# Kernel tuning notes

Measured on AMD Instinct MI355X. Metric: run time of the kernel, lower is better.

The kernel has to match this reference:

```python
import jax, jax.numpy as jnp
import numpy as np

L, D, H, F, V, B, S = 6, 1024, 16, 4096, 32000, 2, 1024
DK = D // H
EPS = 1e-6

def _make_pe(seq, d):
    pos = np.arange(seq)[:, None].astype(np.float32)
    div = np.exp(np.arange(0, d, 2).astype(np.float32) * (-np.log(10000.0) / d))
    pe = np.zeros((seq, d), np.float32)
    pe[:, 0::2] = np.sin(pos * div)
    pe[:, 1::2] = np.cos(pos * div)
    return jnp.asarray(pe)

def setup_inputs() -> dict:
    key = jax.random.key(0)
    ks = jax.random.split(key, 8)
    def xav(k, shape, fi, fo):
        lim = np.sqrt(6.0 / (fi + fo)).astype(np.float32)
        return jax.random.uniform(k, shape, jnp.float32, -lim, lim)
    return {
        "input_ids": jax.random.randint(ks[0], (B, S), 0, V),
        "attention_mask": jnp.ones((B, S), jnp.float32),
        "emb": jax.random.normal(ks[1], (V, D), jnp.float32) * 0.02,
        "pe": _make_pe(S, D),
        "w_q": xav(ks[2], (L, D, D), D, D),
        "w_k": xav(ks[3], (L, D, D), D, D),
        "w_v": xav(ks[4], (L, D, D), D, D),
        "w_o": xav(ks[5], (L, D, D), D, D),
        "b_o": jnp.zeros((L, D), jnp.float32),
        "w1": xav(ks[6], (L, D, F), D, F),
        "b1": jnp.zeros((L, F), jnp.float32),
        "w2": xav(ks[7], (L, F, D), F, D),
        "b2": jnp.zeros((L, D), jnp.float32),
        "ln1_s": jnp.ones((L, D), jnp.float32),
        "ln1_b": jnp.zeros((L, D), jnp.float32),
        "ln2_s": jnp.ones((L, D), jnp.float32),
        "ln2_b": jnp.zeros((L, D), jnp.float32),
        "lnf_s": jnp.ones((D,), jnp.float32),
        "lnf_b": jnp.zeros((D,), jnp.float32),
    }

def _ln(x, s, b):
    m = x.mean(-1, keepdims=True)
    v = jnp.mean((x - m) ** 2, axis=-1, keepdims=True)  # biased var, like torch LayerNorm
    return (x - m) / jnp.sqrt(v + EPS) * s + b

def reference(input_ids, attention_mask, emb, pe, w_q, w_k, w_v, w_o, b_o,
              w1, b1, w2, b2, ln1_s, ln1_b, ln2_s, ln2_b, lnf_s, lnf_b):
    mask = attention_mask[:, None, None, :]          # [B,1,1,S], broadcasts over heads & queries
    x = emb[input_ids] * jnp.sqrt(jnp.float32(D)) + pe[None, :S]   # [B,S,D]

    def heads(h, w):                                 # [B,S,D] -> [B,H,S,DK]
        return (h @ w).reshape(B, S, H, DK).transpose(0, 2, 1, 3)

    def step(x, p):
        wq, wk, wv, wo, bo, W1, B1, W2, B2, s1, c1, s2, c2 = p
        h = _ln(x, s1, c1)                           # pre-norm
        q, k, v = heads(h, wq), heads(h, wk), heads(h, wv)
        scores = jnp.einsum('bhqd,bhkd->bhqk', q, k) / np.sqrt(DK).astype(np.float32)
        scores = jnp.where(mask == 0, -1e9, scores)
        attn = jax.nn.softmax(scores, axis=-1)       # dropout is identity in eval
        out = jnp.einsum('bhqk,bhkd->bhqd', attn, v)
        out = out.transpose(0, 2, 1, 3).reshape(B, S, D) @ wo + bo
        x = x + out
        h2 = _ln(x, s2, c2)
        ff = jax.nn.relu(h2 @ W1 + B1) @ W2 + B2
        return x + ff, None

    x, _ = jax.lax.scan(step, x, (w_q, w_k, w_v, w_o, b_o, w1, b1, w2, b2,
                                  ln1_s, ln1_b, ln2_s, ln2_b))
    return _ln(x, lnf_s, lnf_b)                      # last_hidden_state [B,S,D]
```

## Files before the change

### kernel.cpp

```cpp
#include <hip/hip_runtime.h>
#include <hip/hip_bf16.h>

#define DL 6
#define DD 1024
#define DH 16
#define DF 4096
#define DB 2
#define DS 1024
#define DDK 64

typedef __hip_bfloat16 bf16;
typedef short mfma_t;
typedef mfma_t mfma8 __attribute__((ext_vector_type(8)));
typedef float floatx4 __attribute__((ext_vector_type(4)));

__device__ __forceinline__ float b2f(bf16 v) { return __bfloat162float(v); }
__device__ __forceinline__ bf16 f2b(float v) { return __float2bfloat16(v); }
__device__ __forceinline__ float rd(const void* p, size_t i, int dt) {
  return dt ? b2f(((const bf16*)p)[i]) : ((const float*)p)[i];
}

__device__ __forceinline__ void gld_lds16(const bf16* g, bf16* l) {
  __builtin_amdgcn_global_load_lds(
      (const __attribute__((address_space(1))) unsigned int*)g,
      (__attribute__((address_space(3))) unsigned int*)l, 16, 0, 0);
}

__global__ void detect_dtype(const unsigned* __restrict__ msk, int* __restrict__ flag) {
  if (threadIdx.x == 0) flag[0] = (msk[0] == 0x3F800000u) ? 0 : 1;
}

template <int OP>
__device__ __forceinline__ float block_reduce(float v, float* sm) {
#pragma unroll
  for (int off = 32; off > 0; off >>= 1) {
    float o = __shfl_down(v, off, 64);
    v = OP ? fmaxf(v, o) : v + o;
  }
  if ((threadIdx.x & 63) == 0) sm[threadIdx.x >> 6] = v;
  __syncthreads();
  float r = OP ? fmaxf(fmaxf(sm[0], sm[1]), fmaxf(sm[2], sm[3]))
               : (sm[0] + sm[1]) + (sm[2] + sm[3]);
  __syncthreads();
  return r;
}

__global__ __launch_bounds__(256) void embed_kernel(const int* __restrict__ ids,
                                                    const void* __restrict__ emb,
                                                    const void* __restrict__ pe,
                                                    const int* __restrict__ dflag,
                                                    float* __restrict__ x) {
  const int dt = dflag[0];
  int t = blockIdx.x;
  int id = ids[t];
  int s = t & (DS - 1);
  int c = threadIdx.x * 4;
  float* xo = x + (size_t)t * DD + c;
#pragma unroll
  for (int i = 0; i < 4; ++i)
    xo[i] = rd(emb, (size_t)id * DD + c + i, dt) * 32.0f + rd(pe, (size_t)s * DD + c + i, dt);
}

__global__ __launch_bounds__(256) void ln_kernel(const float* __restrict__ x,
                                                 const void* __restrict__ s,
                                                 const void* __restrict__ b,
                                                 long long poff,
                                                 const int* __restrict__ dflag,
                                                 void* __restrict__ out, int is_final) {
  __shared__ float sm[4];
  const int dt = dflag[0];
  int row = blockIdx.x;
  const float4* xr = (const float4*)(x + (size_t)row * DD);
  float4 v = xr[threadIdx.x];
  float sum = block_reduce<0>(v.x + v.y + v.z + v.w, sm);
  float mean = sum * (1.0f / DD);
  float dx = v.x - mean, dy = v.y - mean, dz = v.z - mean, dw = v.w - mean;
  float ss = block_reduce<0>(dx * dx + dy * dy + dz * dz + dw * dw, sm);
  float rstd = rsqrtf(ss * (1.0f / DD) + 1e-6f);
  int c = threadIdx.x * 4;
  size_t p = (size_t)poff + c;
  float o0 = dx * rstd * rd(s, p + 0, dt) + rd(b, p + 0, dt);
  float o1 = dy * rstd * rd(s, p + 1, dt) + rd(b, p + 1, dt);
  float o2 = dz * rstd * rd(s, p + 2, dt) + rd(b, p + 2, dt);
  float o3 = dw * rstd * rd(s, p + 3, dt) + rd(b, p + 3, dt);
  if (is_final && dt == 0) {
    float* o = (float*)out + (size_t)row * DD + c;
    o[0] = o0; o[1] = o1; o[2] = o2; o[3] = o3;
  } else {
    bf16* o = (bf16*)out + (size_t)row * DD + c;
    o[0] = f2b(o0); o[1] = f2b(o1); o[2] = f2b(o2); o[3] = f2b(o3);
  }
}

__global__ __launch_bounds__(256) void transpose_any(const void* __restrict__ in,
                                                     long long row_off,
                                                     bf16* __restrict__ out,
                                                     int rows, int cols,
                                                     const int* __restrict__ dflag) {
  __shared__ bf16 t[32][33];
  const int dt = dflag[0];
  int c0 = blockIdx.x * 32, r0 = blockIdx.y * 32;
  int tx = threadIdx.x & 31, ty = threadIdx.x >> 5;
#pragma unroll
  for (int i = 0; i < 4; ++i) {
    int r = ty + i * 8;
    size_t idx = (size_t)(row_off + r0 + r) * cols + c0 + tx;
    t[r][tx] = dt ? ((const bf16*)in)[idx] : f2b(((const float*)in)[idx]);
  }
  __syncthreads();
#pragma unroll
  for (int i = 0; i < 4; ++i) {
    int r = ty + i * 8;
    out[(size_t)(c0 + r) * rows + r0 + tx] = t[tx][r];
  }
}

__global__ __launch_bounds__(256) void vtrans_kernel(const bf16* __restrict__ qkv,
                                                     bf16* __restrict__ vt) {
  __shared__ bf16 t[32][33];
  int bh = blockIdx.z;
  const bf16* src = qkv + (size_t)(bh >> 4) * DS * 3072 + 2048 + (bh & 15) * DDK;
  bf16* dst = vt + (size_t)bh * DDK * DS;
  int s0 = blockIdx.x * 32, d0 = blockIdx.y * 32;
  int tx = threadIdx.x & 31, ty = threadIdx.x >> 5;
#pragma unroll
  for (int i = 0; i < 4; ++i) {
    int r = ty + i * 8;
    t[r][tx] = src[(size_t)(s0 + r) * 3072 + d0 + tx];
  }
  __syncthreads();
#pragma unroll
  for (int i = 0; i < 4; ++i) {
    int r = ty + i * 8;
    dst[(size_t)(d0 + r) * DS + s0 + tx] = t[tx][r];
  }
}

#define KVBLK 128
__global__ __launch_bounds__(256) void flash_attn(const bf16* __restrict__ qkv,
                                                  const bf16* __restrict__ vt,
                                                  const void* __restrict__ msk,
                                                  const int* __restrict__ dflag,
                                                  bf16* __restrict__ ao) {
  __shared__ __align__(16) bf16 Qs[64 * 64];
  __shared__ __align__(16) bf16 Ks[KVBLK * 64];
  __shared__ __align__(16) bf16 Vs[64 * KVBLK];
  __shared__ __align__(16) bf16 Ps[4 * 16 * KVBLK];
  __shared__ float Ms[KVBLK];
  __shared__ float Sx[4][16];

  const int tid = threadIdx.x;
  const int lane = tid & 63, wave = tid >> 6;
  const int lane16 = lane & 15, laneq = lane >> 4;
  const int dt = dflag[0];
  const int qt = blockIdx.x, bh = blockIdx.y;
  const int b = bh >> 4, h = bh & 15;
  const int q0 = qt * 64;

  const bf16* Qg = qkv + (size_t)b * DS * 3072 + (size_t)q0 * 3072 + h * 64;
  const bf16* Kg = qkv + (size_t)b * DS * 3072 + 1024 + h * 64;
  const bf16* Vg = vt + (size_t)bh * DDK * DS;

#pragma unroll
  for (int i = 0; i < 2; ++i) {
    int c = tid + i * 256;
    int row = c >> 3, sl = c & 7;
    gld_lds16(Qg + (size_t)row * 3072 + ((sl ^ (row & 7)) << 3), &Qs[c * 8]);
  }
  auto stage = [&](int kv0) {
#pragma unroll
    for (int i = 0; i < 4; ++i) {
      int c = tid + i * 256;
      int row = c >> 3, sl = c & 7;
      gld_lds16(Kg + (size_t)(kv0 + row) * 3072 + ((sl ^ (row & 7)) << 3), &Ks[c * 8]);
    }
#pragma unroll
    for (int i = 0; i < 4; ++i) {
      int c = tid + i * 256;
      int row = c >> 4, sl = c & 15;
      gld_lds16(Vg + (size_t)row * DS + kv0 + ((sl ^ (row & 7)) << 3), &Vs[c * 8]);
    }
    if (tid < KVBLK) Ms[tid] = rd(msk, (size_t)b * DS + kv0 + tid, dt);
  };

  stage(0);
  __syncthreads();

  mfma8 bq[2];
  {
    int qrow = wave * 16 + lane16;
#pragma unroll
    for (int ks = 0; ks < 2; ++ks)
      bq[ks] = *(const mfma8*)(&Qs[qrow * 64 + (((laneq + ks * 4) ^ (qrow & 7)) << 3)]);
  }

  floatx4 acc_o[4];
#pragma unroll
  for (int d = 0; d < 4; ++d) { floatx4 z = {0.f, 0.f, 0.f, 0.f}; acc_o[d] = z; }
  float m_run = -1e30f, l_run = 0.f;

  for (int kv = 0; kv < DS / KVBLK; ++kv) {
    floatx4 s[8];
#pragma unroll
    for (int t = 0; t < 8; ++t) { floatx4 z = {0.f, 0.f, 0.f, 0.f}; s[t] = z; }
#pragma unroll
    for (int ks = 0; ks < 2; ++ks)
#pragma unroll
      for (int t = 0; t < 8; ++t) {
        int krow = t * 16 + lane16;
        mfma8 a = *(const mfma8*)(&Ks[krow * 64 + (((laneq + ks * 4) ^ (krow & 7)) << 3)]);
        s[t] = __builtin_amdgcn_mfma_f32_16x16x32_bf16(a, bq[ks], s[t], 0, 0, 0);
      }
    float pmax = -1e30f;
#pragma unroll
    for (int t = 0; t < 8; ++t) {
      float4 mk = *(const float4*)(&Ms[t * 16 + laneq * 4]);
#pragma unroll
      for (int r = 0; r < 4; ++r) {
        float sv = ((&mk.x)[r] == 0.f) ? -1e9f : s[t][r] * 0.125f;
        s[t][r] = sv;
        pmax = fmaxf(pmax, sv);
      }
    }
    pmax = fmaxf(pmax, __shfl_xor(pmax, 16, 64));
    pmax = fmaxf(pmax, __shfl_xor(pmax, 32, 64));
    float m_new = fmaxf(m_run, pmax);
    float scal = __expf(m_run - m_new);
    float lsum = 0.f;
#pragma unroll
    for (int t = 0; t < 8; ++t)
#pragma unroll
      for (int r = 0; r < 4; ++r) {
        float p = __expf(s[t][r] - m_new);
        s[t][r] = p;
        lsum += p;
      }
    lsum += __shfl_xor(lsum, 16, 64);
    lsum += __shfl_xor(lsum, 32, 64);
    l_run = l_run * scal + lsum;
    m_run = m_new;
    if (laneq == 0) Sx[wave][lane16] = scal;
    {
      int rowb = (wave * 16 + lane16) * 2 * KVBLK;
#pragma unroll
      for (int t = 0; t < 8; ++t) {
        int off = (t * 32 + laneq * 8) ^ ((lane16 & 7) << 4);
        union { bf16 v[4]; uint2 u; } pk;
        pk.v[0] = f2b(s[t][0]); pk.v[1] = f2b(s[t][1]);
        pk.v[2] = f2b(s[t][2]); pk.v[3] = f2b(s[t][3]);
        *(uint2*)((char*)&Ps[0] + rowb + off) = pk.u;
      }
    }
    float4 sc4 = *(const float4*)(&Sx[wave][laneq * 4]);
#pragma unroll
    for (int d = 0; d < 4; ++d)
#pragma unroll
      for (int r = 0; r < 4; ++r) acc_o[d][r] *= (&sc4.x)[r];
#pragma unroll
    for (int ks = 0; ks < 4; ++ks) {
      mfma8 pa = *(const mfma8*)((char*)&Ps[0] + (wave * 16 + lane16) * 2 * KVBLK +
                                 ((ks * 64 + laneq * 16) ^ ((lane16 & 7) << 4)));
#pragma unroll
      for (int d = 0; d < 4; ++d) {
        int drow = d * 16 + lane16;
        mfma8 vb = *(const mfma8*)((char*)&Vs[0] + drow * 2 * KVBLK +
                                   ((ks * 64 + laneq * 16) ^ ((drow & 7) << 4)));
        acc_o[d] = __builtin_amdgcn_mfma_f32_16x16x32_bf16(pa, vb, acc_o[d], 0, 0, 0);
      }
    }
    __syncthreads();
    if (kv + 1 < DS / KVBLK) {
      stage((kv + 1) * KVBLK);
      __syncthreads();
    }
  }

  if (laneq == 0) Sx[wave][lane16] = l_run;
  float4 l4 = *(const float4*)(&Sx[wave][laneq * 4]);
#pragma unroll
  for (int r = 0; r < 4; ++r) {
    float inv = 1.f / (&l4.x)[r];
    int q = q0 + wave * 16 + laneq * 4 + r;
    size_t base = ((size_t)b * DS + q) * DD + h * 64;
#pragma unroll
    for (int d = 0; d < 4; ++d) ao[base + d * 16 + lane16] = f2b(acc_o[d][r] * inv);
  }
}

enum { EPI_BF16 = 0, EPI_BIAS_RELU = 1, EPI_ACC_ATOMIC = 2, EPI_SCORES = 3 };

template <int NT, int WM_, int WN_, int TM, int TN, int EPI>
__global__ __launch_bounds__(256) void gemm_bt(
    const bf16* __restrict__ A, int lda, long long zsa,
    const bf16* __restrict__ Bt, int ldb, long long zsb,
    void* __restrict__ C, int ldc, long long zsc,
    int K, const void* __restrict__ aux, long long aoff, float scale,
    const int* __restrict__ dflag) {
  constexpr int MT = 128, BK = 32;
  constexpr int SM = MT / WM_, SN = NT / WN_;
  constexpr int nsA = (MT * BK / 8) / 256;
  constexpr int nsB = (NT * BK / 8) / 256;
  __shared__ __align__(16) bf16 As[2][MT * BK];
  __shared__ __align__(16) bf16 Bs[2][NT * BK];
  const int tid = threadIdx.x;
  const int lane = tid & 63, wave = tid >> 6;
  const int lane16 = lane & 15, laneq = lane >> 4;
  const int wm = wave / WN_, wn = wave % WN_;
  const int dt = dflag[0];
  const long long z = blockIdx.z;
  A += z * zsa;
  Bt += z * zsb;
  const int m0 = blockIdx.x * MT, n0 = blockIdx.y * NT;

  floatx4 acc[TM][TN];
#pragma unroll
  for (int i = 0; i < TM; ++i)
#pragma unroll
    for (int j = 0; j < TN; ++j) {
      floatx4 zz = {0.f, 0.f, 0.f, 0.f};
      acc[i][j] = zz;
    }

  auto stage = [&](int buf, int k0) {
#pragma unroll
    for (int i = 0; i < nsA; ++i) {
      int c = tid + i * 256;
      int row = c >> 2, kk = (c & 3) << 3;
      gld_lds16(A + (size_t)(m0 + row) * lda + k0 + kk,
                &As[buf][(size_t)(wave * 64 + i * 256) * 8]);
    }
#pragma unroll
    for (int i = 0; i < nsB; ++i) {
      int c = tid + i * 256;
      int row = c >> 2, kk = (c & 3) << 3;
      gld_lds16(Bt + (size_t)(n0 + row) * ldb + k0 + kk,
                &Bs[buf][(size_t)(wave * 64 + i * 256) * 8]);
    }
  };

  stage(0, 0);
  __syncthreads();

  int cur = 0;
  for (int k0 = 0; k0 < K; k0 += BK, cur ^= 1) {
    if (k0 + BK < K) stage(cur ^ 1, k0 + BK);
    mfma8 af[TM], bfr[TN];
#pragma unroll
    for (int i = 0; i < TM; ++i)
      af[i] = *(const mfma8*)(&As[cur][(wm * SM + i * 16 + lane16) * BK + laneq * 8]);
#pragma unroll
    for (int j = 0; j < TN; ++j)
      bfr[j] = *(const mfma8*)(&Bs[cur][(wn * SN + j * 16 + lane16) * BK + laneq * 8]);
#pragma unroll
    for (int i = 0; i < TM; ++i)
#pragma unroll
      for (int j = 0; j < TN; ++j)
        acc[i][j] = __builtin_amdgcn_mfma_f32_16x16x32_bf16(af[i], bfr[j], acc[i][j], 0, 0, 0);
    __syncthreads();
  }

#pragma unroll
  for (int i = 0; i < TM; ++i) {
    const int rb = m0 + wm * SM + i * 16 + laneq * 4;
#pragma unroll
    for (int j = 0; j < TN; ++j) {
      const int col = n0 + wn * SN + j * 16 + lane16;
#pragma unroll
      for (int r = 0; r < 4; ++r) {
        const size_t idx = (size_t)(rb + r) * ldc + col;
        float v = acc[i][j][r];
        if constexpr (EPI == EPI_BF16) {
          ((bf16*)C)[(size_t)(z * zsc) + idx] = f2b(v);
        } else if constexpr (EPI == EPI_BIAS_RELU) {
          v += rd(aux, (size_t)(aoff + col), dt);
          ((bf16*)C)[idx] = f2b(fmaxf(v, 0.f));
        } else if constexpr (EPI == EPI_ACC_ATOMIC) {
          if (z == 0) v += rd(aux, (size_t)(aoff + col), dt);
          atomicAdd((float*)C + idx, v);
        } else {
          v *= scale;
          if (rd(aux, (size_t)(aoff + col), dt) == 0.f) v = -1e9f;
          ((float*)C)[(size_t)(z * zsc) + idx] = v;
        }
      }
    }
  }
}

extern "C" void kernel_launch(void* const* d_in, const int* in_sizes, int n_in,
                              void* d_out, int out_size, void* d_ws, size_t ws_size,
                              hipStream_t stream) {
  const int* ids   = (const int*)d_in[0];
  const void* msk  = d_in[1];
  const void* emb  = d_in[2];
  const void* pe   = d_in[3];
  const void* w_q  = d_in[4];
  const void* w_k  = d_in[5];
  const void* w_v  = d_in[6];
  const void* w_o  = d_in[7];
  const void* b_o  = d_in[8];
  const void* w1   = d_in[9];
  const void* b1   = d_in[10];
  const void* w2   = d_in[11];
  const void* b2   = d_in[12];
  const void* ln1s = d_in[13];
  const void* ln1b = d_in[14];
  const void* ln2s = d_in[15];
  const void* ln2b = d_in[16];
  const void* lnfs = d_in[17];
  const void* lnfb = d_in[18];

  char* ws = (char*)d_ws;
  float* x   = (float*)(ws + 0);
  bf16* qkv  = (bf16*)(ws + 8388608);
  bf16* h    = (bf16*)(ws + 20971520);
  bf16* ao   = (bf16*)(ws + 25165824);
  bf16* vt   = (bf16*)(ws + 29360128);
  bf16* mid  = (bf16*)(ws + 33554432);
  bf16* wT   = (bf16*)(ws + 50331648);
  int* flag  = (int*)(ws + 58720256);

  dim3 blk(256);
  detect_dtype<<<1, 64, 0, stream>>>((const unsigned*)msk, flag);
  embed_kernel<<<DB * DS, blk, 0, stream>>>(ids, emb, pe, flag, x);

  for (int l = 0; l < DL; ++l) {
    const long long lo = (long long)l * DD;
    const long long lw = (long long)l * DD;

    ln_kernel<<<DB * DS, blk, 0, stream>>>(x, ln1s, ln1b, lo, flag, h, 0);

    transpose_any<<<dim3(32, 32), blk, 0, stream>>>(w_q, lw, wT, DD, DD, flag);
    transpose_any<<<dim3(32, 32), blk, 0, stream>>>(w_k, lw, wT + DD * DD, DD, DD, flag);
    transpose_any<<<dim3(32, 32), blk, 0, stream>>>(w_v, lw, wT + 2 * DD * DD, DD, DD, flag);
    gemm_bt<128, 2, 2, 4, 4, EPI_BF16><<<dim3(16, 24, 1), blk, 0, stream>>>(
        h, DD, 0, wT, DD, 0, qkv, 3072, 0, DD, nullptr, 0, 1.f, flag);

    vtrans_kernel<<<dim3(32, 2, 32), blk, 0, stream>>>(qkv, vt);
    flash_attn<<<dim3(DS / 64, DB * DH), blk, 0, stream>>>(qkv, vt, msk, flag, ao);

    transpose_any<<<dim3(32, 32), blk, 0, stream>>>(w_o, lw, wT, DD, DD, flag);
    gemm_bt<128, 2, 2, 4, 4, EPI_ACC_ATOMIC><<<dim3(16, 8, 2), blk, 0, stream>>>(
        ao, DD, 512, wT, DD, 512, x, DD, 0, 512, b_o, lo, 1.f, flag);

    ln_kernel<<<DB * DS, blk, 0, stream>>>(x, ln2s, ln2b, lo, flag, h, 0);

    transpose_any<<<dim3(128, 32), blk, 0, stream>>>(w1, lw, wT, DD, DF, flag);
    gemm_bt<128, 2, 2, 4, 4, EPI_BIAS_RELU><<<dim3(16, 32, 1), blk, 0, stream>>>(
        h, DD, 0, wT, DD, 0, mid, DF, 0, DD, b1, (long long)l * DF, 1.f, flag);

    transpose_any<<<dim3(32, 128), blk, 0, stream>>>(w2, (long long)l * DF, wT, DF, DD, flag);
    gemm_bt<128, 2, 2, 4, 4, EPI_ACC_ATOMIC><<<dim3(16, 8, 2), blk, 0, stream>>>(
        mid, DF, 2048, wT, DF, 2048, x, DD, 0, 2048, b2, lo, 1.f, flag);
  }

  ln_kernel<<<DB * DS, blk, 0, stream>>>(x, lnfs, lnfb, 0, flag, d_out, 1);
}
```

Before: 1.776 ms.

## Batch all weight transposes upfront, raise split-K, add MFMA priority hints

All per-layer weight transposes are replaced by three batched launches before the layer loop, each writing into its own dedicated workspace region. This removes 30 small kernel launches and lets the transposes run at full-GPU parallelism, at the cost of a larger workspace. The output-projection and FFN2 GEMMs double their split-K factor from 2 to 4 to launch more blocks, which also doubles the atomic accumulation traffic into x. Flash attention wraps its MFMA sections in s_setprio hints to favour matrix issue.

```diff
diff --git a/kernel.cpp b/kernel.cpp
--- a/kernel.cpp
+++ b/kernel.cpp
@@ -92,26 +92,56 @@
   }
 }
 
-__global__ __launch_bounds__(256) void transpose_any(const void* __restrict__ in,
-                                                     long long row_off,
-                                                     bf16* __restrict__ out,
-                                                     int rows, int cols,
-                                                     const int* __restrict__ dflag) {
+__global__ __launch_bounds__(256) void transpose_sq(const void* __restrict__ w_q,
+                                                    const void* __restrict__ w_k,
+                                                    const void* __restrict__ w_v,
+                                                    const void* __restrict__ w_o,
+                                                    bf16* __restrict__ out,
+                                                    const int* __restrict__ dflag) {
   __shared__ bf16 t[32][33];
   const int dt = dflag[0];
+  const int z = blockIdx.z, l = z >> 2, which = z & 3;
+  const void* in = which == 0 ? w_q : which == 1 ? w_k : which == 2 ? w_v : w_o;
+  const long long row_off = (long long)l * DD;
+  bf16* o = out + (size_t)z * DD * DD;
   int c0 = blockIdx.x * 32, r0 = blockIdx.y * 32;
   int tx = threadIdx.x & 31, ty = threadIdx.x >> 5;
 #pragma unroll
   for (int i = 0; i < 4; ++i) {
     int r = ty + i * 8;
-    size_t idx = (size_t)(row_off + r0 + r) * cols + c0 + tx;
+    size_t idx = (size_t)(row_off + r0 + r) * DD + c0 + tx;
     t[r][tx] = dt ? ((const bf16*)in)[idx] : f2b(((const float*)in)[idx]);
   }
   __syncthreads();
 #pragma unroll
   for (int i = 0; i < 4; ++i) {
     int r = ty + i * 8;
-    out[(size_t)(c0 + r) * rows + r0 + tx] = t[tx][r];
+    o[(size_t)(c0 + r) * DD + r0 + tx] = t[tx][r];
+  }
+}
+
+__global__ __launch_bounds__(256) void transpose_rect(const void* __restrict__ in,
+                                                      bf16* __restrict__ out,
+                                                      int R, int C,
+                                                      const int* __restrict__ dflag) {
+  __shared__ bf16 t[32][33];
+  const int dt = dflag[0];
+  const int l = blockIdx.z;
+  const long long row_off = (long long)l * R;
+  bf16* o = out + (size_t)l * R * C;
+  int c0 = blockIdx.x * 32, r0 = blockIdx.y * 32;
+  int tx = threadIdx.x & 31, ty = threadIdx.x >> 5;
+#pragma unroll
+  for (int i = 0; i < 4; ++i) {
+    int r = ty + i * 8;
+    size_t idx = (size_t)(row_off + r0 + r) * C + c0 + tx;
+    t[r][tx] = dt ? ((const bf16*)in)[idx] : f2b(((const float*)in)[idx]);
+  }
+  __syncthreads();
+#pragma unroll
+  for (int i = 0; i < 4; ++i) {
+    int r = ty + i * 8;
+    o[(size_t)(c0 + r) * R + r0 + tx] = t[tx][r];
   }
 }
 
@@ -203,6 +233,7 @@
     floatx4 s[8];
 #pragma unroll
     for (int t = 0; t < 8; ++t) { floatx4 z = {0.f, 0.f, 0.f, 0.f}; s[t] = z; }
+    __builtin_amdgcn_s_setprio(1);
 #pragma unroll
     for (int ks = 0; ks < 2; ++ks)
 #pragma unroll
@@ -211,6 +242,7 @@
         mfma8 a = *(const mfma8*)(&Ks[krow * 64 + (((laneq + ks * 4) ^ (krow & 7)) << 3)]);
         s[t] = __builtin_amdgcn_mfma_f32_16x16x32_bf16(a, bq[ks], s[t], 0, 0, 0);
       }
+    __builtin_amdgcn_s_setprio(0);
     float pmax = -1e30f;
 #pragma unroll
     for (int t = 0; t < 8; ++t) {
@@ -256,6 +288,7 @@
     for (int d = 0; d < 4; ++d)
 #pragma unroll
       for (int r = 0; r < 4; ++r) acc_o[d][r] *= (&sc4.x)[r];
+    __builtin_amdgcn_s_setprio(1);
 #pragma unroll
     for (int ks = 0; ks < 4; ++ks) {
       mfma8 pa = *(const mfma8*)((char*)&Ps[0] + (wave * 16 + lane16) * 2 * KVBLK +
@@ -268,6 +301,7 @@
         acc_o[d] = __builtin_amdgcn_mfma_f32_16x16x32_bf16(pa, vb, acc_o[d], 0, 0, 0);
       }
     }
+    __builtin_amdgcn_s_setprio(0);
     __syncthreads();
     if (kv + 1 < DS / KVBLK) {
       stage((kv + 1) * KVBLK);
@@ -412,46 +446,50 @@
 
   char* ws = (char*)d_ws;
   float* x   = (float*)(ws + 0);
-  bf16* qkv  = (bf16*)(ws + 8388608);
-  bf16* h    = (bf16*)(ws + 20971520);
-  bf16* ao   = (bf16*)(ws + 25165824);
-  bf16* vt   = (bf16*)(ws + 29360128);
-  bf16* mid  = (bf16*)(ws + 33554432);
-  bf16* wT   = (bf16*)(ws + 50331648);
-  int* flag  = (int*)(ws + 58720256);
+  bf16* qkv  = (bf16*)(ws + (8u << 20));
+  bf16* h    = (bf16*)(ws + (20u << 20));
+  bf16* ao   = (bf16*)(ws + (24u << 20));
+  bf16* vt   = (bf16*)(ws + (28u << 20));
+  bf16* mid  = (bf16*)(ws + (32u << 20));
+  int* flag  = (int*)(ws + (48u << 20));
+  bf16* wTsq = (bf16*)(ws + (64u << 20));
+  bf16* w1T  = (bf16*)(ws + (112u << 20));
+  bf16* w2T  = (bf16*)(ws + (160u << 20));
 
   dim3 blk(256);
   detect_dtype<<<1, 64, 0, stream>>>((const unsigned*)msk, flag);
+
+  transpose_sq<<<dim3(32, 32, DL * 4), blk, 0, stream>>>(w_q, w_k, w_v, w_o, wTsq, flag);
+  transpose_rect<<<dim3(128, 32, DL), blk, 0, stream>>>(w1, w1T, DD, DF, flag);
+  transpose_rect<<<dim3(32, 128, DL), blk, 0, stream>>>(w2, w2T, DF, DD, flag);
+
   embed_kernel<<<DB * DS, blk, 0, stream>>>(ids, emb, pe, flag, x);
 
   for (int l = 0; l < DL; ++l) {
     const long long lo = (long long)l * DD;
-    const long long lw = (long long)l * DD;
+    bf16* wq_l = wTsq + (size_t)(l * 4) * DD * DD;
+    bf16* wo_l = wTsq + (size_t)(l * 4 + 3) * DD * DD;
+    bf16* w1_l = w1T + (size_t)l * DF * DD;
+    bf16* w2_l = w2T + (size_t)l * DD * DF;
 
     ln_kernel<<<DB * DS, blk, 0, stream>>>(x, ln1s, ln1b, lo, flag, h, 0);
 
-    transpose_any<<<dim3(32, 32), blk, 0, stream>>>(w_q, lw, wT, DD, DD, flag);
-    transpose_any<<<dim3(32, 32), blk, 0, stream>>>(w_k, lw, wT + DD * DD, DD, DD, flag);
-    transpose_any<<<dim3(32, 32), blk, 0, stream>>>(w_v, lw, wT + 2 * DD * DD, DD, DD, flag);
     gemm_bt<128, 2, 2, 4, 4, EPI_BF16><<<dim3(16, 24, 1), blk, 0, stream>>>(
-        h, DD, 0, wT, DD, 0, qkv, 3072, 0, DD, nullptr, 0, 1.f, flag);
+        h, DD, 0, wq_l, DD, 0, qkv, 3072, 0, DD, nullptr, 0, 1.f, flag);
 
     vtrans_kernel<<<dim3(32, 2, 32), blk, 0, stream>>>(qkv, vt);
     flash_attn<<<dim3(DS / 64, DB * DH), blk, 0, stream>>>(qkv, vt, msk, flag, ao);
 
-    transpose_any<<<dim3(32, 32), blk, 0, stream>>>(w_o, lw, wT, DD, DD, flag);
-    gemm_bt<128, 2, 2, 4, 4, EPI_ACC_ATOMIC><<<dim3(16, 8, 2), blk, 0, stream>>>(
-        ao, DD, 512, wT, DD, 512, x, DD, 0, 512, b_o, lo, 1.f, flag);
+    gemm_bt<128, 2, 2, 4, 4, EPI_ACC_ATOMIC><<<dim3(16, 8, 4), blk, 0, stream>>>(
+        ao, DD, 256, wo_l, DD, 256, x, DD, 0, 256, b_o, lo, 1.f, flag);
 
     ln_kernel<<<DB * DS, blk, 0, stream>>>(x, ln2s, ln2b, lo, flag, h, 0);
 
-    transpose_any<<<dim3(128, 32), blk, 0, stream>>>(w1, lw, wT, DD, DF, flag);
     gemm_bt<128, 2, 2, 4, 4, EPI_BIAS_RELU><<<dim3(16, 32, 1), blk, 0, stream>>>(
-        h, DD, 0, wT, DD, 0, mid, DF, 0, DD, b1, (long long)l * DF, 1.f, flag);
-
-    transpose_any<<<dim3(32, 128), blk, 0, stream>>>(w2, (long long)l * DF, wT, DF, DD, flag);
-    gemm_bt<128, 2, 2, 4, 4, EPI_ACC_ATOMIC><<<dim3(16, 8, 2), blk, 0, stream>>>(
-        mid, DF, 2048, wT, DF, 2048, x, DD, 0, 2048, b2, lo, 1.f, flag);
+        h, DD, 0, w1_l, DD, 0, mid, DF, 0, DD, b1, (long long)l * DF, 1.f, flag);
+
+    gemm_bt<128, 2, 2, 4, 4, EPI_ACC_ATOMIC><<<dim3(16, 8, 4), blk, 0, stream>>>(
+        mid, DF, 1024, w2_l, DF, 1024, x, DD, 0, 1024, b2, lo, 1.f, flag);
   }
 
   ln_kernel<<<DB * DS, blk, 0, stream>>>(x, lnfs, lnfb, 0, flag, d_out, 1);
```

Result: no change. 1.770 ms (-0.3%).
